# Kernel optimization log

Hardware: AMD Instinct MI355X
Metric: run time of the kernel (lower is better)

Reference implementation:

```python
import jax, jax.numpy as jnp
import numpy as np

B, F, DIN, DOUT = 4096, 64, 256, 256

def setup_inputs() -> dict:
    key = jax.random.key(0)
    k1, k2, k3 = jax.random.split(key, 3)
    init_max = 1.0 / DIN ** 0.5
    x = jax.random.normal(k1, (B, F, DIN), dtype=jnp.float32)
    weight = jax.random.uniform(k2, (F, DIN, DOUT), dtype=jnp.float32, minval=-init_max, maxval=init_max)
    b = jax.random.uniform(k3, (F, DOUT), dtype=jnp.float32, minval=-init_max, maxval=init_max)
    return {"x": x, "weight": weight, "b": b}

def reference(x, weight, b) -> jnp.ndarray:
    # Per-feature grouped linear: for each feature f, out[:, f] = x[:, f] @ weight[f] + b[f]
    # Equivalent to (x[..., None] * weight[None]).sum(axis=2) + bias, but as batched GEMM.
    out = jnp.einsum('bfi,fio->bfo', x, weight)
    return out + b[None, :, :]
```

## Files before the change

### kernel.cpp

```cpp
#include <hip/hip_runtime.h>
#include <stdint.h>

#define BATCH 4096
#define FEAT  64
#define DIN   256
#define DOUT  256

typedef __attribute__((ext_vector_type(8))) short  short8;
typedef __attribute__((ext_vector_type(4))) float  float4v;
typedef __attribute__((ext_vector_type(4))) unsigned int uint4v;

__device__ __forceinline__ unsigned int pack_bf16(float lo, float hi) {
    unsigned int ulo = __builtin_bit_cast(unsigned int, lo) + 0x8000u;
    unsigned int uhi = __builtin_bit_cast(unsigned int, hi) + 0x8000u;
    return __builtin_amdgcn_perm(uhi, ulo, 0x07060302u);
}

#define A_STRIDE 264

__global__ __launch_bounds__(256)
void wprep_kernel(const float* __restrict__ w, unsigned short* __restrict__ wb) {
    const int blk = blockIdx.x;
    const int n   = threadIdx.x;
    const float* src = w + (size_t)blk * 8 * DOUT + n;
    float v0 = src[0 * DOUT], v1 = src[1 * DOUT];
    float v2 = src[2 * DOUT], v3 = src[3 * DOUT];
    float v4 = src[4 * DOUT], v5 = src[5 * DOUT];
    float v6 = src[6 * DOUT], v7 = src[7 * DOUT];
    uint4v p;
    p.x = pack_bf16(v0, v1);
    p.y = pack_bf16(v2, v3);
    p.z = pack_bf16(v4, v5);
    p.w = pack_bf16(v6, v7);
    *(uint4v*)(wb + ((size_t)blk * DOUT + n) * 8) = p;
}

__device__ __forceinline__ void stage_x_tile(const float* __restrict__ x,
                                             unsigned short* Alds,
                                             int b0, int f, int tid) {
    const float* xb = x + (size_t)(b0 * FEAT + f) * DIN;
    #pragma unroll
    for (int i = 0; i < 8; ++i) {
        int chunk = tid + 256 * i;
        int row   = chunk >> 5;
        int c8    = (chunk & 31) * 8;
        const float* g = xb + row * (FEAT * DIN) + c8;
        float4v a0 = *(const float4v*)g;
        float4v a1 = *(const float4v*)(g + 4);
        uint4v p;
        p.x = pack_bf16(a0.x, a0.y);
        p.y = pack_bf16(a0.z, a0.w);
        p.z = pack_bf16(a1.x, a1.y);
        p.w = pack_bf16(a1.z, a1.w);
        *(uint4v*)&Alds[row * A_STRIDE + c8] = p;
    }
}

__global__ __launch_bounds__(256, 3)
void nlinear_kernel(const float* __restrict__ x,
                    const short8* __restrict__ wb,
                    const float* __restrict__ bias,
                    float* __restrict__ out) {
    __shared__ __align__(16) unsigned short Alds[64 * A_STRIDE];

    const int tid = threadIdx.x;
    const int f   = blockIdx.x & 63;
    const int mb  = blockIdx.x >> 6;
    const int b0  = mb * 64;

    stage_x_tile(x, Alds, b0, f, tid);
    __syncthreads();

    const int lane = tid & 63;
    const int wv   = tid >> 6;
    const int q    = lane >> 4;
    const int l16  = lane & 15;
    const int n0   = wv * 64;

    float4v acc[4][4];
    #pragma unroll
    for (int s = 0; s < 4; ++s) {
        float bv = bias[f * DOUT + n0 + s * 16 + l16];
        #pragma unroll
        for (int mi = 0; mi < 4; ++mi)
            acc[mi][s] = (float4v){bv, bv, bv, bv};
    }

    const short8* wbase = wb + ((size_t)f * 32) * DOUT + n0 + l16;
    const unsigned short* albase = Alds + l16 * A_STRIDE + q * 8;

    #pragma unroll 2
    for (int it = 0; it < 8; ++it) {
        const int kb = it * 32;
        const short8* wk = wbase + (size_t)(it * 4 + q) * DOUT;

        short8 bfrag[4];
        #pragma unroll
        for (int s = 0; s < 4; ++s)
            bfrag[s] = wk[s * 16];

        short8 afrag[4];
        #pragma unroll
        for (int mi = 0; mi < 4; ++mi)
            afrag[mi] = *(const short8*)(albase + mi * 16 * A_STRIDE + kb);

        #pragma unroll
        for (int mi = 0; mi < 4; ++mi)
            #pragma unroll
            for (int s = 0; s < 4; ++s)
                acc[mi][s] = __builtin_amdgcn_mfma_f32_16x16x32_bf16(
                    afrag[mi], bfrag[s], acc[mi][s], 0, 0, 0);
    }

    float* ob = out + (size_t)(b0 * FEAT + f) * DOUT + n0;
    #pragma unroll
    for (int mi = 0; mi < 4; ++mi) {
        #pragma unroll
        for (int r = 0; r < 4; ++r) {
            int m = mi * 16 + q * 4 + r;
            float* orow = ob + m * (FEAT * DOUT);
            #pragma unroll
            for (int s = 0; s < 4; ++s)
                orow[s * 16 + l16] = acc[mi][s][r];
        }
    }
}

__global__ __launch_bounds__(256, 2)
void nlinear_fallback(const float* __restrict__ x,
                      const float* __restrict__ w,
                      const float* __restrict__ bias,
                      float* __restrict__ out) {
    __shared__ __align__(16) unsigned short Alds[64 * A_STRIDE];

    const int tid = threadIdx.x;
    const int f   = blockIdx.x & 63;
    const int mb  = blockIdx.x >> 6;
    const int b0  = mb * 64;

    stage_x_tile(x, Alds, b0, f, tid);
    __syncthreads();

    const int lane = tid & 63;
    const int wv   = tid >> 6;
    const int q    = lane >> 4;
    const int l16  = lane & 15;
    const int n0   = wv * 64;

    float4v acc[4][4];
    #pragma unroll
    for (int s = 0; s < 4; ++s) {
        float bv = bias[f * DOUT + n0 + s * 16 + l16];
        #pragma unroll
        for (int mi = 0; mi < 4; ++mi)
            acc[mi][s] = (float4v){bv, bv, bv, bv};
    }

    const float* wp = w + (size_t)f * (DIN * DOUT) + n0 + q * 8 * DOUT + l16;
    const unsigned short* albase = Alds + l16 * A_STRIDE + q * 8;

    #pragma unroll 2
    for (int it = 0; it < 8; ++it) {
        const int kb = it * 32;
        const float* wk = wp + kb * DOUT;

        short8 bfrag[4];
        #pragma unroll
        for (int s = 0; s < 4; ++s) {
            float v0 = wk[0 * DOUT + s * 16];
            float v1 = wk[1 * DOUT + s * 16];
            float v2 = wk[2 * DOUT + s * 16];
            float v3 = wk[3 * DOUT + s * 16];
            float v4 = wk[4 * DOUT + s * 16];
            float v5 = wk[5 * DOUT + s * 16];
            float v6 = wk[6 * DOUT + s * 16];
            float v7 = wk[7 * DOUT + s * 16];
            uint4v p;
            p.x = pack_bf16(v0, v1);
            p.y = pack_bf16(v2, v3);
            p.z = pack_bf16(v4, v5);
            p.w = pack_bf16(v6, v7);
            bfrag[s] = __builtin_bit_cast(short8, p);
        }

        short8 afrag[4];
        #pragma unroll
        for (int mi = 0; mi < 4; ++mi)
            afrag[mi] = *(const short8*)(albase + mi * 16 * A_STRIDE + kb);

        #pragma unroll
        for (int mi = 0; mi < 4; ++mi)
            #pragma unroll
            for (int s = 0; s < 4; ++s)
                acc[mi][s] = __builtin_amdgcn_mfma_f32_16x16x32_bf16(
                    afrag[mi], bfrag[s], acc[mi][s], 0, 0, 0);
    }

    float* ob = out + (size_t)(b0 * FEAT + f) * DOUT + n0;
    #pragma unroll
    for (int mi = 0; mi < 4; ++mi) {
        #pragma unroll
        for (int r = 0; r < 4; ++r) {
            int m = mi * 16 + q * 4 + r;
            float* orow = ob + m * (FEAT * DOUT);
            #pragma unroll
            for (int s = 0; s < 4; ++s)
                orow[s * 16 + l16] = acc[mi][s][r];
        }
    }
}

extern "C" void kernel_launch(void* const* d_in, const int* in_sizes, int n_in,
                              void* d_out, int out_size, void* d_ws, size_t ws_size,
                              hipStream_t stream) {
    const float* x    = (const float*)d_in[0];
    const float* w    = (const float*)d_in[1];
    const float* bias = (const float*)d_in[2];
    float* out = (float*)d_out;

    const size_t WB_BYTES = (size_t)FEAT * DIN * DOUT * sizeof(unsigned short);

    if (d_ws != nullptr && ws_size >= WB_BYTES) {
        unsigned short* wbuf = (unsigned short*)d_ws;
        wprep_kernel<<<dim3(FEAT * (DIN / 8)), dim3(256), 0, stream>>>(w, wbuf);
        nlinear_kernel<<<dim3(FEAT * (BATCH / 64)), dim3(256), 0, stream>>>(
            x, (const short8*)wbuf, bias, out);
    } else {
        nlinear_fallback<<<dim3(FEAT * (BATCH / 64)), dim3(256), 0, stream>>>(
            x, w, bias, out);
    }
}
```

Baseline: 453.0 us.

## Load x fragments directly from global into registers, drop LDS staging

The main kernel no longer stages the 64-row x tile into shared memory behind a barrier. Each wave now loads its own A fragments straight from global memory into registers, converts them to bf16 on the fly, and prefetches the next k-slice while the current MFMAs run. The wave tiling changes from 4 waves × 64 columns to a 2×2 grid of 32 rows × 128 columns, so each wave reloads fewer A rows but reads more B fragments. This removes the LDS write/read and the __syncthreads, at the cost of less coalesced x loads (16 rows per wave instruction) and higher register pressure from 16 accumulators plus the prefetch buffers.

```diff
diff --git a/kernel.cpp b/kernel.cpp
--- a/kernel.cpp
+++ b/kernel.cpp
@@ -16,7 +16,14 @@
     return __builtin_amdgcn_perm(uhi, ulo, 0x07060302u);
 }
 
-#define A_STRIDE 264
+__device__ __forceinline__ short8 pack8(float4v lo, float4v hi) {
+    uint4v p;
+    p.x = pack_bf16(lo.x, lo.y);
+    p.y = pack_bf16(lo.z, lo.w);
+    p.z = pack_bf16(hi.x, hi.y);
+    p.w = pack_bf16(hi.z, hi.w);
+    return __builtin_bit_cast(short8, p);
+}
 
 __global__ __launch_bounds__(256)
 void wprep_kernel(const float* __restrict__ w, unsigned short* __restrict__ wb) {
@@ -35,97 +42,105 @@
     *(uint4v*)(wb + ((size_t)blk * DOUT + n) * 8) = p;
 }
 
-__device__ __forceinline__ void stage_x_tile(const float* __restrict__ x,
-                                             unsigned short* Alds,
-                                             int b0, int f, int tid) {
-    const float* xb = x + (size_t)(b0 * FEAT + f) * DIN;
-    #pragma unroll
-    for (int i = 0; i < 8; ++i) {
-        int chunk = tid + 256 * i;
-        int row   = chunk >> 5;
-        int c8    = (chunk & 31) * 8;
-        const float* g = xb + row * (FEAT * DIN) + c8;
-        float4v a0 = *(const float4v*)g;
-        float4v a1 = *(const float4v*)(g + 4);
-        uint4v p;
-        p.x = pack_bf16(a0.x, a0.y);
-        p.y = pack_bf16(a0.z, a0.w);
-        p.z = pack_bf16(a1.x, a1.y);
-        p.w = pack_bf16(a1.z, a1.w);
-        *(uint4v*)&Alds[row * A_STRIDE + c8] = p;
-    }
-}
-
 __global__ __launch_bounds__(256, 3)
 void nlinear_kernel(const float* __restrict__ x,
                     const short8* __restrict__ wb,
                     const float* __restrict__ bias,
                     float* __restrict__ out) {
-    __shared__ __align__(16) unsigned short Alds[64 * A_STRIDE];
-
-    const int tid = threadIdx.x;
-    const int f   = blockIdx.x & 63;
-    const int mb  = blockIdx.x >> 6;
-    const int b0  = mb * 64;
-
-    stage_x_tile(x, Alds, b0, f, tid);
-    __syncthreads();
+    const int tid  = threadIdx.x;
+    const int f    = blockIdx.x & 63;
+    const int mb   = blockIdx.x >> 6;
+    const int b0   = mb * 64;
 
     const int lane = tid & 63;
     const int wv   = tid >> 6;
+    const int wm   = wv >> 1;
+    const int wn   = wv & 1;
     const int q    = lane >> 4;
     const int l16  = lane & 15;
-    const int n0   = wv * 64;
-
-    float4v acc[4][4];
-    #pragma unroll
-    for (int s = 0; s < 4; ++s) {
+    const int n0   = wn * 128;
+    const int m0   = b0 + wm * 32;
+
+    float4v acc[2][8];
+    #pragma unroll
+    for (int s = 0; s < 8; ++s) {
         float bv = bias[f * DOUT + n0 + s * 16 + l16];
-        #pragma unroll
-        for (int mi = 0; mi < 4; ++mi)
-            acc[mi][s] = (float4v){bv, bv, bv, bv};
-    }
-
-    const short8* wbase = wb + ((size_t)f * 32) * DOUT + n0 + l16;
-    const unsigned short* albase = Alds + l16 * A_STRIDE + q * 8;
-
-    #pragma unroll 2
-    for (int it = 0; it < 8; ++it) {
-        const int kb = it * 32;
-        const short8* wk = wbase + (size_t)(it * 4 + q) * DOUT;
-
-        short8 bfrag[4];
-        #pragma unroll
-        for (int s = 0; s < 4; ++s)
-            bfrag[s] = wk[s * 16];
-
-        short8 afrag[4];
-        #pragma unroll
-        for (int mi = 0; mi < 4; ++mi)
-            afrag[mi] = *(const short8*)(albase + mi * 16 * A_STRIDE + kb);
-
-        #pragma unroll
-        for (int mi = 0; mi < 4; ++mi)
-            #pragma unroll
-            for (int s = 0; s < 4; ++s)
-                acc[mi][s] = __builtin_amdgcn_mfma_f32_16x16x32_bf16(
-                    afrag[mi], bfrag[s], acc[mi][s], 0, 0, 0);
-    }
-
-    float* ob = out + (size_t)(b0 * FEAT + f) * DOUT + n0;
-    #pragma unroll
-    for (int mi = 0; mi < 4; ++mi) {
+        acc[0][s] = (float4v){bv, bv, bv, bv};
+        acc[1][s] = (float4v){bv, bv, bv, bv};
+    }
+
+    const float* xr0 = x + ((size_t)(m0 + l16) * FEAT + f) * DIN + q * 8;
+    const float* xr1 = xr0 + (size_t)16 * FEAT * DIN;
+    const short8* wbase = wb + (size_t)f * 32 * DOUT + n0 + l16;
+
+    float4v xA0 = *(const float4v*)(xr0);
+    float4v xA1 = *(const float4v*)(xr0 + 4);
+    float4v xA2 = *(const float4v*)(xr1);
+    float4v xA3 = *(const float4v*)(xr1 + 4);
+
+    #pragma unroll
+    for (int t = 0; t < 4; ++t) {
+        const int itA = 2 * t, itB = 2 * t + 1;
+
+        float4v xB0 = *(const float4v*)(xr0 + itB * 32);
+        float4v xB1 = *(const float4v*)(xr0 + itB * 32 + 4);
+        float4v xB2 = *(const float4v*)(xr1 + itB * 32);
+        float4v xB3 = *(const float4v*)(xr1 + itB * 32 + 4);
+
+        {
+            short8 af0 = pack8(xA0, xA1);
+            short8 af1 = pack8(xA2, xA3);
+            const short8* wk = wbase + (size_t)(itA * 4 + q) * DOUT;
+            short8 bf[8];
+            #pragma unroll
+            for (int s = 0; s < 8; ++s) bf[s] = wk[s * 16];
+            #pragma unroll
+            for (int s = 0; s < 8; ++s) {
+                acc[0][s] = __builtin_amdgcn_mfma_f32_16x16x32_bf16(
+                    af0, bf[s], acc[0][s], 0, 0, 0);
+                acc[1][s] = __builtin_amdgcn_mfma_f32_16x16x32_bf16(
+                    af1, bf[s], acc[1][s], 0, 0, 0);
+            }
+        }
+
+        if (t < 3) {
+            xA0 = *(const float4v*)(xr0 + (itB + 1) * 32);
+            xA1 = *(const float4v*)(xr0 + (itB + 1) * 32 + 4);
+            xA2 = *(const float4v*)(xr1 + (itB + 1) * 32);
+            xA3 = *(const float4v*)(xr1 + (itB + 1) * 32 + 4);
+        }
+
+        {
+            short8 af0 = pack8(xB0, xB1);
+            short8 af1 = pack8(xB2, xB3);
+            const short8* wk = wbase + (size_t)(itB * 4 + q) * DOUT;
+            short8 bf[8];
+            #pragma unroll
+            for (int s = 0; s < 8; ++s) bf[s] = wk[s * 16];
+            #pragma unroll
+            for (int s = 0; s < 8; ++s) {
+                acc[0][s] = __builtin_amdgcn_mfma_f32_16x16x32_bf16(
+                    af0, bf[s], acc[0][s], 0, 0, 0);
+                acc[1][s] = __builtin_amdgcn_mfma_f32_16x16x32_bf16(
+                    af1, bf[s], acc[1][s], 0, 0, 0);
+            }
+        }
+    }
+
+    float* ob = out + ((size_t)m0 * FEAT + f) * DOUT + n0;
+    #pragma unroll
+    for (int mi = 0; mi < 2; ++mi) {
         #pragma unroll
         for (int r = 0; r < 4; ++r) {
-            int m = mi * 16 + q * 4 + r;
-            float* orow = ob + m * (FEAT * DOUT);
-            #pragma unroll
-            for (int s = 0; s < 4; ++s)
+            float* orow = ob + (size_t)(mi * 16 + q * 4 + r) * (FEAT * DOUT);
+            #pragma unroll
+            for (int s = 0; s < 8; ++s)
                 orow[s * 16 + l16] = acc[mi][s][r];
         }
     }
 }
 
+#define A_STRIDE 264
 __global__ __launch_bounds__(256, 2)
 void nlinear_fallback(const float* __restrict__ x,
                       const float* __restrict__ w,
@@ -138,7 +153,24 @@
     const int mb  = blockIdx.x >> 6;
     const int b0  = mb * 64;
 
-    stage_x_tile(x, Alds, b0, f, tid);
+    {
+        const float* xb = x + (size_t)(b0 * FEAT + f) * DIN;
+        #pragma unroll
+        for (int i = 0; i < 8; ++i) {
+            int chunk = tid + 256 * i;
+            int row   = chunk >> 5;
+            int c8    = (chunk & 31) * 8;
+            const float* g = xb + row * (FEAT * DIN) + c8;
+            float4v a0 = *(const float4v*)g;
+            float4v a1 = *(const float4v*)(g + 4);
+            uint4v p;
+            p.x = pack_bf16(a0.x, a0.y);
+            p.y = pack_bf16(a0.z, a0.w);
+            p.z = pack_bf16(a1.x, a1.y);
+            p.w = pack_bf16(a1.z, a1.w);
+            *(uint4v*)&Alds[row * A_STRIDE + c8] = p;
+        }
+    }
     __syncthreads();
 
     const int lane = tid & 63;
```

New measurement: 509.5 us. +12.5%, slower.
